# Kernel tuning notes

Hardware: AMD Instinct MI355X
Metric: run time of the kernel (lower is better)

## Reference

```python
import jax, jax.numpy as jnp
import numpy as np

VOCAB = 32000
D_MODEL = 512
SEQ_TABLE = 2048
EPS = 1e-5


def layer_norm(x, gamma, beta):
    mu = jnp.mean(x, axis=-1, keepdims=True)
    var = jnp.mean(jnp.square(x - mu), axis=-1, keepdims=True)
    return (x - mu) * jax.lax.rsqrt(var + EPS) * gamma + beta


def setup_inputs() -> dict:
    key = jax.random.key(0)
    ks = jax.random.split(key, 12)
    s = 0.02
    d, h, V = D_MODEL, 4 * D_MODEL, VOCAB
    return {
        "x": jax.random.randint(ks[0], (4, 2048), 0, V, dtype=jnp.int64),
        "word_emb": jax.random.normal(ks[1], (V, d), jnp.float32) * s,
        "pos_emb": jax.random.normal(ks[2], (SEQ_TABLE, d), jnp.float32) * s,
        "Wq": jax.random.normal(ks[3], (d, d), jnp.float32) * s,
        "Wk": jax.random.normal(ks[4], (d, d), jnp.float32) * s,
        "Wv": jax.random.normal(ks[5], (d, d), jnp.float32) * s,
        "g1": jnp.ones((d,), jnp.float32),
        "b1": jnp.zeros((d,), jnp.float32),
        "w_ffn1": jax.random.normal(ks[6], (h, d), jnp.float32) * s,
        "b_ffn1": jnp.zeros((h,), jnp.float32),
        "w_ffn2": jax.random.normal(ks[7], (d, h), jnp.float32) * s,
        "b_ffn2": jnp.zeros((d,), jnp.float32),
        "g2": jnp.ones((d,), jnp.float32),
        "b2": jnp.zeros((d,), jnp.float32),
        "w_vocab": jax.random.normal(ks[8], (V, d), jnp.float32) * s,
        "b_vocab": jnp.zeros((V,), jnp.float32),
    }


def reference(x, word_emb, pos_emb, Wq, Wk, Wv, g1, b1,
              w_ffn1, b_ffn1, w_ffn2, b_ffn2, g2, b2, w_vocab, b_vocab):
    B, S = x.shape
    d_k = Wq.shape[0]
    # embeddings: word + learned positional
    emb = word_emb[x] + pos_emb[jnp.arange(S)][None, :, :]  # [B,S,d]
    # single-head causal attention (torch Linear: y = x @ W.T)
    Q = emb @ Wq.T
    K = emb @ Wk.T
    V = emb @ Wv.T
    scores = jnp.einsum('bqd,bkd->bqk', Q, K) / jnp.sqrt(jnp.float32(d_k))
    causal = jnp.tril(jnp.ones((S, S), bool))
    scores = jnp.where(causal[None], scores, -jnp.inf)
    attn = jax.nn.softmax(scores, axis=-1)
    context = jnp.einsum('bqk,bkd->bqd', attn, V)
    out1 = layer_norm(emb + context, g1, b1)
    ffn = jax.nn.relu(out1 @ w_ffn1.T + b_ffn1) @ w_ffn2.T + b_ffn2
    final = layer_norm(out1 + ffn, g2, b2)
    return final @ w_vocab.T + b_vocab  # [B,S,V]
```

## Files before the change

kernel.cpp:

```cpp
#include <hip/hip_runtime.h>
#include <hip/hip_bf16.h>

typedef __bf16 bf16;
typedef __attribute__((ext_vector_type(4))) __bf16 bf16x4;
typedef __attribute__((ext_vector_type(8))) __bf16 bf16x8;
typedef __attribute__((ext_vector_type(4))) float f32x4;

__device__ inline void gload_lds16(const bf16* g, bf16* l) {
    __builtin_amdgcn_global_load_lds(
        (const __attribute__((address_space(1))) void*)g,
        (__attribute__((address_space(3))) void*)l, 16, 0, 0);
}

struct CvtArgs {
    const float* src[6];
    bf16* dst[6];
    long n4[6];
    float scale[6];
};
__global__ void cvt_all(CvtArgs a) {
    int j = blockIdx.y;
    const float* __restrict__ src = a.src[j];
    bf16* __restrict__ dst = a.dst[j];
    long n4 = a.n4[j];
    float sc = a.scale[j];
    long i = (long)blockIdx.x * blockDim.x + threadIdx.x;
    long stride = (long)gridDim.x * blockDim.x;
    for (; i < n4; i += stride) {
        float4 v = ((const float4*)src)[i];
        bf16x4 o = { (bf16)(v.x * sc), (bf16)(v.y * sc), (bf16)(v.z * sc), (bf16)(v.w * sc) };
        ((bf16x4*)dst)[i] = o;
    }
}

__global__ void embed_kernel(const int* __restrict__ x, const float* __restrict__ we,
                             const float* __restrict__ pe, float* __restrict__ emb_f,
                             bf16* __restrict__ emb_b) {
    int row = blockIdx.x;
    int c   = threadIdx.x;
    int tok = x[row];
    int s   = row & 2047;
    float4 w = ((const float4*)we)[(long)tok * 128 + c];
    float4 p = ((const float4*)pe)[(long)s * 128 + c];
    float4 e = { w.x + p.x, w.y + p.y, w.z + p.z, w.w + p.w };
    ((float4*)emb_f)[(long)row * 128 + c] = e;
    bf16x4 eb = { (bf16)e.x, (bf16)e.y, (bf16)e.z, (bf16)e.w };
    ((bf16x4*)emb_b)[(long)row * 128 + c] = eb;
}

template<bool WF32>
__global__ void ln_kernel(const float* __restrict__ a, const float* __restrict__ bres,
                          const float* __restrict__ g, const float* __restrict__ bb,
                          float* __restrict__ of, bf16* __restrict__ ob) {
    int row = blockIdx.x;
    int t   = threadIdx.x;
    float4 xa = ((const float4*)a)[(long)row * 128 + t];
    float4 xb = ((const float4*)bres)[(long)row * 128 + t];
    float4 xv = { xa.x + xb.x, xa.y + xb.y, xa.z + xb.z, xa.w + xb.w };
    float s  = xv.x + xv.y + xv.z + xv.w;
    float sq = xv.x * xv.x + xv.y * xv.y + xv.z * xv.z + xv.w * xv.w;
    #pragma unroll
    for (int o = 32; o > 0; o >>= 1) {
        s  += __shfl_xor(s, o);
        sq += __shfl_xor(sq, o);
    }
    __shared__ float rs[2], rq[2];
    int wid = t >> 6;
    if ((t & 63) == 0) { rs[wid] = s; rq[wid] = sq; }
    __syncthreads();
    s = rs[0] + rs[1]; sq = rq[0] + rq[1];
    float mu   = s * (1.0f / 512.0f);
    float var  = sq * (1.0f / 512.0f) - mu * mu;
    float rstd = rsqrtf(var + 1e-5f);
    float4 gv = ((const float4*)g)[t];
    float4 bv = ((const float4*)bb)[t];
    float4 y = { (xv.x - mu) * rstd * gv.x + bv.x,
                 (xv.y - mu) * rstd * gv.y + bv.y,
                 (xv.z - mu) * rstd * gv.z + bv.z,
                 (xv.w - mu) * rstd * gv.w + bv.w };
    if (WF32) ((float4*)of)[(long)row * 128 + t] = y;
    bf16x4 yb = { (bf16)y.x, (bf16)y.y, (bf16)y.z, (bf16)y.w };
    ((bf16x4*)ob)[(long)row * 128 + t] = yb;
}

__global__ void softmax_causal(const float* __restrict__ sc, bf16* __restrict__ pr) {
    int row = blockIdx.x;
    int z = row >> 11, q = row & 2047;
    const float* srow = sc + ((long)z * 2048 + q) * 2048;
    bf16*        prow = pr + ((long)z * 2048 + q) * 2048;
    int t = threadIdx.x;
    float v[8];
    int c0 = t * 8;
    if (t <= (q >> 3)) {
        float4 v0 = ((const float4*)srow)[t * 2];
        float4 v1 = ((const float4*)srow)[t * 2 + 1];
        v[0] = v0.x; v[1] = v0.y; v[2] = v0.z; v[3] = v0.w;
        v[4] = v1.x; v[5] = v1.y; v[6] = v1.z; v[7] = v1.w;
    } else {
        #pragma unroll
        for (int j = 0; j < 8; j++) v[j] = -1e30f;
    }
    float mx = -1e30f;
    #pragma unroll
    for (int j = 0; j < 8; j++) {
        if (c0 + j > q) v[j] = -1e30f;
        mx = fmaxf(mx, v[j]);
    }
    int lane = t & 63, wid = t >> 6;
    #pragma unroll
    for (int o = 32; o > 0; o >>= 1) mx = fmaxf(mx, __shfl_xor(mx, o));
    __shared__ float redm[4], reds[4];
    if (lane == 0) redm[wid] = mx;
    __syncthreads();
    mx = fmaxf(fmaxf(redm[0], redm[1]), fmaxf(redm[2], redm[3]));
    float p[8]; float sum = 0.f;
    #pragma unroll
    for (int j = 0; j < 8; j++) {
        p[j] = (c0 + j <= q) ? __expf(v[j] - mx) : 0.f;
        sum += p[j];
    }
    #pragma unroll
    for (int o = 32; o > 0; o >>= 1) sum += __shfl_xor(sum, o);
    if (lane == 0) reds[wid] = sum;
    __syncthreads();
    sum = reds[0] + reds[1] + reds[2] + reds[3];
    float inv = 1.0f / sum;
    int wlim = ((q >> 7) + 1) * 128;
    if (c0 < wlim) {
        bf16x8 o;
        #pragma unroll
        for (int j = 0; j < 8; j++) o[j] = (bf16)(p[j] * inv);
        *(bf16x8*)&prow[c0] = o;
    }
}

enum { EPI_F32 = 0, EPI_BF16 = 1, EPI_VT = 2, EPI_BIAS_RELU_BF16 = 3, EPI_BIAS_F32 = 4,
       EPI_QKV = 5, EPI_BIAS_F32_NT = 6 };
enum { ZB_BATCH = 0 };

template<int EPI, bool CAUSAL_SKIP, bool CAUSAL_K, bool XCD, int ZMODE>
__global__ __launch_bounds__(256)
void gemm_bt(const bf16* __restrict__ A, const bf16* __restrict__ B,
             float* __restrict__ Cf, bf16* __restrict__ Cb,
             const float* __restrict__ bias, float scale,
             int M, int N, int K, int Krow, long sA, long sB, long sC) {
    int br, bc;
    if (XCD) {
        int nwg = gridDim.x * gridDim.y;
        int lin = blockIdx.y * gridDim.x + blockIdx.x;
        lin = (lin & 7) * (nwg >> 3) + (lin >> 3);
        br = lin / gridDim.x; bc = lin - br * gridDim.x;
    } else { br = blockIdx.y; bc = blockIdx.x; }
    int z = blockIdx.z;
    A += (long)z * sA; B += (long)z * sB; Cf += (long)z * sC;
    if (CAUSAL_SKIP && bc > br) return;
    int Kext = CAUSAL_K ? min(K, (br + 1) * 128) : K;
    __shared__ bf16 As[128 * 64];
    __shared__ bf16 Bs[128 * 64];
    int tid = threadIdx.x;
    int lane = tid & 63, wid = tid >> 6;
    int wm = (wid >> 1) * 64, wn = (wid & 1) * 64;
    f32x4 acc[4][4] = {};
    int rowA0 = br * 128, colB0 = bc * 128;
    int rsub = lane >> 3;
    int csub = ((lane & 7) ^ rsub) * 8;
    int rdsw = (lane & 7) * 8;
    for (int kt = 0; kt < Kext; kt += 64) {
        const bf16* Ag = A + (long)rowA0 * Krow + kt;
        const bf16* Bg = B + (long)colB0 * Krow + kt;
        #pragma unroll
        for (int i = 0; i < 4; i++) {
            int seg = wid * 4 + i;
            int r = seg * 8 + rsub;
            gload_lds16(&Ag[(long)r * Krow + csub], &As[seg * 512]);
            gload_lds16(&Bg[(long)r * Krow + csub], &Bs[seg * 512]);
        }
        __syncthreads();
        #pragma unroll
        for (int kk = 0; kk < 2; kk++) {
            bf16x8 af[4], bfr[4];
            int ko = (kk * 32 + (lane >> 4) * 8) ^ rdsw;
            #pragma unroll
            for (int m = 0; m < 4; m++) af[m]  = *(const bf16x8*)&As[(wm + m * 16 + (lane & 15)) * 64 + ko];
            #pragma unroll
            for (int n = 0; n < 4; n++) bfr[n] = *(const bf16x8*)&Bs[(wn + n * 16 + (lane & 15)) * 64 + ko];
            #pragma unroll
            for (int m = 0; m < 4; m++)
                #pragma unroll
                for (int n = 0; n < 4; n++)
                    acc[m][n] = __builtin_amdgcn_mfma_f32_16x16x32_bf16(af[m], bfr[n], acc[m][n], 0, 0, 0);
        }
        __syncthreads();
    }
    #pragma unroll
    for (int m = 0; m < 4; m++) {
        #pragma unroll
        for (int n = 0; n < 4; n++) {
            #pragma unroll
            for (int j = 0; j < 4; j++) {
                int row = rowA0 + wm + m * 16 + (lane >> 4) * 4 + j;
                int col = colB0 + wn + n * 16 + (lane & 15);
                float v = acc[m][n][j];
                if (EPI == EPI_F32) {
                    Cf[(long)row * N + col] = v;
                } else if (EPI == EPI_BF16) {
                    Cb[(long)row * N + col] = (bf16)(v * scale);
                } else if (EPI == EPI_VT) {
                    int b = row >> 11, k = row & 2047;
                    Cb[((long)b * 512 + col) * 2048 + k] = (bf16)v;
                } else if (EPI == EPI_BIAS_RELU_BF16) {
                    float y = fmaxf(v + bias[col], 0.0f);
                    Cb[(long)row * N + col] = (bf16)y;
                } else if (EPI == EPI_BIAS_F32) {
                    Cf[(long)row * N + col] = v + bias[col];
                }
            }
        }
    }
}

template<int EPI, bool XCD, bool CSKIP, int BANDW, int NT>
__global__ __launch_bounds__(512)
void gemm256(const bf16* __restrict__ A, const bf16* __restrict__ B,
             float* __restrict__ Cf, bf16* __restrict__ Cb,
             const float* __restrict__ bias, int N, int K,
             long sA, long sB, long sC) {
    int br, bc;
    if (XCD) {
        int nwg = gridDim.x * gridDim.y;
        int lin = blockIdx.y * gridDim.x + blockIdx.x;
        lin = (lin & 7) * (nwg >> 3) + (lin >> 3);
        if (BANDW > 0) {
            int per = BANDW * gridDim.y;
            int band = lin / per, w2 = lin - band * per;
            br = w2 / BANDW; bc = band * BANDW + (w2 - br * BANDW);
        } else {
            br = lin / gridDim.x; bc = lin - br * gridDim.x;
        }
    } else { br = blockIdx.y; bc = blockIdx.x; }
    if (CSKIP && bc > br) return;
    int z = blockIdx.z;
    A  += (long)z * sA;
    B  += (long)z * sB;
    Cf += (long)z * sC;
    __shared__ bf16 lds[2][2][256 * 64];
    int tid = threadIdx.x;
    int lane = tid & 63, wid = tid >> 6;
    int wm2 = wid >> 2, wn4 = wid & 3;
    long rowA0 = (long)br * 256, colB0 = (long)bc * 256;
    int rsub = lane >> 3;
    int csw  = ((lane & 7) ^ rsub) * 8;
    int l15 = lane & 15;
    int rdxor = (lane & 7) << 3;
    int kbase = (lane >> 4) * 8;
    const bf16* Abase = A + rowA0 * K;
    const bf16* Bbase = B + colB0 * K;
    f32x4 acc[8][4] = {};

    auto stage = [&](int t) {
        int buf = t & 1;
        const bf16* Ag = Abase + t * 64;
        const bf16* Bg = Bbase + t * 64;
        #pragma unroll
        for (int i = 0; i < 4; i++) {
            int seg = wid * 4 + i;
            long r = seg * 8 + rsub;
            gload_lds16(&Ag[r * K + csw], &lds[buf][0][seg * 512]);
        }
        #pragma unroll
        for (int i = 0; i < 4; i++) {
            int seg = wid * 4 + i;
            long r = seg * 8 + rsub;
            gload_lds16(&Bg[r * K + csw], &lds[buf][1][seg * 512]);
        }
    };

    stage(0);
    stage(1);

    for (int t = 0; t < NT; t++) {
        int buf = t & 1;
        if (t == NT - 1) asm volatile("s_waitcnt vmcnt(0)" ::: "memory");
        else             asm volatile("s_waitcnt vmcnt(8)" ::: "memory");
        __builtin_amdgcn_s_barrier();
        const bf16* As = lds[buf][0];
        const bf16* Bs = lds[buf][1];
        bf16x8 bfr[2][4], af[2][4];
        #pragma unroll
        for (int kk = 0; kk < 2; kk++)
            #pragma unroll
            for (int n = 0; n < 4; n++) {
                int r = wn4 * 64 + n * 16 + l15;
                bfr[kk][n] = *(const bf16x8*)&Bs[r * 64 + ((kk * 32 + kbase) ^ rdxor)];
            }
        #pragma unroll
        for (int kk = 0; kk < 2; kk++)
            #pragma unroll
            for (int m = 0; m < 4; m++) {
                int r = wm2 * 128 + m * 16 + l15;
                af[kk][m] = *(const bf16x8*)&As[r * 64 + ((kk * 32 + kbase) ^ rdxor)];
            }
        __builtin_amdgcn_s_setprio(1);
        #pragma unroll
        for (int kk = 0; kk < 2; kk++)
            #pragma unroll
            for (int m = 0; m < 4; m++)
                #pragma unroll
                for (int n = 0; n < 4; n++)
                    acc[m][n] = __builtin_amdgcn_mfma_f32_16x16x32_bf16(af[kk][m], bfr[kk][n], acc[m][n], 0, 0, 0);
        __builtin_amdgcn_s_setprio(0);
        #pragma unroll
        for (int kk = 0; kk < 2; kk++)
            #pragma unroll
            for (int m = 0; m < 4; m++) {
                int r = wm2 * 128 + 64 + m * 16 + l15;
                af[kk][m] = *(const bf16x8*)&As[r * 64 + ((kk * 32 + kbase) ^ rdxor)];
            }
        asm volatile("s_waitcnt lgkmcnt(0)" ::: "memory");
        __builtin_amdgcn_sched_barrier(0);
        __builtin_amdgcn_s_barrier();
        if (t + 2 < NT) stage(t + 2);
        __builtin_amdgcn_s_setprio(1);
        #pragma unroll
        for (int kk = 0; kk < 2; kk++)
            #pragma unroll
            for (int m = 0; m < 4; m++)
                #pragma unroll
                for (int n = 0; n < 4; n++)
                    acc[4 + m][n] = __builtin_amdgcn_mfma_f32_16x16x32_bf16(af[kk][m], bfr[kk][n], acc[4 + m][n], 0, 0, 0);
        __builtin_amdgcn_s_setprio(0);
    }

    if constexpr (EPI == EPI_QKV) {
        int region = (int)(colB0 >> 9);
        if (region < 2) {
            bf16* dst = Cb + (long)region * (8192L * 512);
            int cb = ((int)colB0 & 511) + wn4 * 64;
            #pragma unroll
            for (int m = 0; m < 8; m++)
                #pragma unroll
                for (int n = 0; n < 4; n++)
                    #pragma unroll
                    for (int j = 0; j < 4; j++) {
                        long row = rowA0 + wm2 * 128 + m * 16 + (lane >> 4) * 4 + j;
                        int c = cb + n * 16 + l15;
                        dst[row * 512 + c] = (bf16)acc[m][n][j];
                    }
        } else {
            bf16* vtb = Cb + 2L * 8192 * 512;
            int cb = ((int)colB0 - 1024) + wn4 * 64;
            #pragma unroll
            for (int m = 0; m < 8; m++)
                #pragma unroll
                for (int n = 0; n < 4; n++) {
                    long k0 = rowA0 + wm2 * 128 + m * 16 + (lane >> 4) * 4;
                    long b = k0 >> 11, k = k0 & 2047;
                    int c = cb + n * 16 + l15;
                    bf16x4 pk = { (bf16)acc[m][n][0], (bf16)acc[m][n][1],
                                  (bf16)acc[m][n][2], (bf16)acc[m][n][3] };
                    *(bf16x4*)&vtb[(b * 512 + c) * 2048 + k] = pk;
                }
        }
    } else {
        #pragma unroll
        for (int m = 0; m < 8; m++) {
            #pragma unroll
            for (int n = 0; n < 4; n++) {
                #pragma unroll
                for (int j = 0; j < 4; j++) {
                    long row = rowA0 + wm2 * 128 + m * 16 + (lane >> 4) * 4 + j;
                    long col = colB0 + wn4 * 64 + n * 16 + l15;
                    float v = acc[m][n][j];
                    if (EPI == EPI_BIAS_F32) {
                        Cf[row * N + col] = v + bias[col];
                    } else if (EPI == EPI_BIAS_F32_NT) {
                        __builtin_nontemporal_store(v + bias[col], &Cf[row * N + col]);
                    } else if (EPI == EPI_BIAS_RELU_BF16) {
                        Cb[row * N + col] = (bf16)fmaxf(v + bias[col], 0.0f);
                    } else if (EPI == EPI_F32) {
                        Cf[row * N + col] = v;
                    }
                }
            }
        }
    }
}

template<int BANDB>
__global__ __launch_bounds__(256)
void gemm128v(const bf16* __restrict__ A, const bf16* __restrict__ B,
              float* __restrict__ C, const float* __restrict__ bias,
              int N, int K) {
    const int NBR = 64;
    const int NT  = 8;
    int nwg = gridDim.x;
    int lin = blockIdx.x;
    lin = (lin & 7) * (nwg >> 3) + (lin >> 3);
    int per = BANDB * NBR;
    int band = lin / per, w2 = lin - band * per;
    int br = w2 / BANDB, bc = band * BANDB + (w2 - br * BANDB);

    __shared__ bf16 lds[2][2][128 * 64];
    int tid = threadIdx.x;
    int lane = tid & 63, wid = tid >> 6;
    int wm = (wid >> 1) * 64, wn = (wid & 1) * 64;
    int rsub = lane >> 3;
    int csub = ((lane & 7) ^ rsub) * 8;
    int rdsw = (lane & 7) * 8;
    long rowA0 = (long)br * 128, colB0 = (long)bc * 128;
    const bf16* Abase = A + rowA0 * K;
    const bf16* Bbase = B + colB0 * K;
    f32x4 acc[4][4] = {};

    auto stage = [&](int t) {
        int buf = t & 1;
        const bf16* Ag = Abase + t * 64;
        const bf16* Bg = Bbase + t * 64;
        #pragma unroll
        for (int i = 0; i < 4; i++) {
            int seg = wid * 4 + i;
            long r = seg * 8 + rsub;
            gload_lds16(&Ag[r * K + csub], &lds[buf][0][seg * 512]);
        }
        #pragma unroll
        for (int i = 0; i < 4; i++) {
            int seg = wid * 4 + i;
            long r = seg * 8 + rsub;
            gload_lds16(&Bg[r * K + csub], &lds[buf][1][seg * 512]);
        }
    };

    stage(0);
    stage(1);

    for (int t = 0; t < NT; t++) {
        int buf = t & 1;
        if (t == NT - 1) asm volatile("s_waitcnt vmcnt(0)" ::: "memory");
        else             asm volatile("s_waitcnt vmcnt(8)" ::: "memory");
        __builtin_amdgcn_s_barrier();
        const bf16* As = lds[buf][0];
        const bf16* Bs = lds[buf][1];
        __builtin_amdgcn_s_setprio(1);
        #pragma unroll
        for (int kk = 0; kk < 2; kk++) {
            bf16x8 af[4], bfr[4];
            int ko = (kk * 32 + (lane >> 4) * 8) ^ rdsw;
            #pragma unroll
            for (int m = 0; m < 4; m++) af[m]  = *(const bf16x8*)&As[(wm + m * 16 + (lane & 15)) * 64 + ko];
            #pragma unroll
            for (int n = 0; n < 4; n++) bfr[n] = *(const bf16x8*)&Bs[(wn + n * 16 + (lane & 15)) * 64 + ko];
            #pragma unroll
            for (int m = 0; m < 4; m++)
                #pragma unroll
                for (int n = 0; n < 4; n++)
                    acc[m][n] = __builtin_amdgcn_mfma_f32_16x16x32_bf16(af[m], bfr[n], acc[m][n], 0, 0, 0);
        }
        __builtin_amdgcn_s_setprio(0);
        asm volatile("s_waitcnt lgkmcnt(0)" ::: "memory");
        __builtin_amdgcn_sched_barrier(0);
        __builtin_amdgcn_s_barrier();
        if (t + 2 < NT) stage(t + 2);
    }

    #pragma unroll
    for (int m = 0; m < 4; m++) {
        #pragma unroll
        for (int n = 0; n < 4; n++) {
            int col = (int)colB0 + wn + n * 16 + (lane & 15);
            float bcol = bias[col];
            #pragma unroll
            for (int j = 0; j < 4; j++) {
                long row = rowA0 + wm + m * 16 + (lane >> 4) * 4 + j;
                __builtin_nontemporal_store(acc[m][n][j] + bcol, &C[row * N + col]);
            }
        }
    }
}

extern "C" void kernel_launch(void* const* d_in, const int* in_sizes, int n_in,
                              void* d_out, int out_size, void* d_ws, size_t ws_size,
                              hipStream_t stream) {
    const int*   x       = (const int*)d_in[0];
    const float* word_emb = (const float*)d_in[1];
    const float* pos_emb  = (const float*)d_in[2];
    const float* Wq = (const float*)d_in[3];
    const float* Wk = (const float*)d_in[4];
    const float* Wv = (const float*)d_in[5];
    const float* g1 = (const float*)d_in[6];
    const float* b1 = (const float*)d_in[7];
    const float* w_ffn1 = (const float*)d_in[8];
    const float* b_ffn1 = (const float*)d_in[9];
    const float* w_ffn2 = (const float*)d_in[10];
    const float* b_ffn2 = (const float*)d_in[11];
    const float* g2 = (const float*)d_in[12];
    const float* b2 = (const float*)d_in[13];
    const float* w_vocab = (const float*)d_in[14];
    const float* b_vocab = (const float*)d_in[15];
    float* out = (float*)d_out;

    char* w = (char*)d_ws;
    auto alloc = [&](size_t bytes) { char* p = w; w += (bytes + 255) & ~255ULL; return p; };
    bf16* wqb   = (bf16*)alloc(512 * 512 * 2);
    bf16* wkb   = (bf16*)alloc(512 * 512 * 2);
    bf16* wvb   = (bf16*)alloc(512 * 512 * 2);
    bf16* w1b   = (bf16*)alloc(2048 * 512 * 2);
    bf16* w2b   = (bf16*)alloc(512 * 2048 * 2);
    bf16* wvocb = (bf16*)alloc((size_t)32000 * 512 * 2);
    float* embf = (float*)alloc((size_t)8192 * 512 * 4);
    bf16* embb  = (bf16*)alloc((size_t)8192 * 512 * 2);
    bf16* qb    = (bf16*)alloc((size_t)8192 * 512 * 2);
    bf16* kb    = (bf16*)alloc((size_t)8192 * 512 * 2);
    bf16* vt    = (bf16*)alloc((size_t)8192 * 512 * 2);
    float* scores = (float*)alloc((size_t)4 * 2048 * 2048 * 4);
    bf16* probs = (bf16*)alloc((size_t)4 * 2048 * 2048 * 2);
    float* ctx  = (float*)alloc((size_t)8192 * 512 * 4);
    float* out1f = (float*)alloc((size_t)8192 * 512 * 4);
    float* ffn2f = (float*)alloc((size_t)8192 * 512 * 4);
    bf16* ffn1b = (bf16*)scores;
    bf16* out1b = kb;
    bf16* finalb = embb;

    const float qscale = 0.044194173824159216f;

    CvtArgs ca;
    ca.src[0] = Wq;      ca.dst[0] = wqb;   ca.n4[0] = 512 * 512 / 4;          ca.scale[0] = qscale;
    ca.src[1] = Wk;      ca.dst[1] = wkb;   ca.n4[1] = 512 * 512 / 4;          ca.scale[1] = 1.0f;
    ca.src[2] = Wv;      ca.dst[2] = wvb;   ca.n4[2] = 512 * 512 / 4;          ca.scale[2] = 1.0f;
    ca.src[3] = w_ffn1;  ca.dst[3] = w1b;   ca.n4[3] = 2048 * 512 / 4;         ca.scale[3] = 1.0f;
    ca.src[4] = w_ffn2;  ca.dst[4] = w2b;   ca.n4[4] = 512 * 2048 / 4;         ca.scale[4] = 1.0f;
    ca.src[5] = w_vocab; ca.dst[5] = wvocb; ca.n4[5] = (long)32000 * 512 / 4;  ca.scale[5] = 1.0f;
    cvt_all<<<dim3(256, 6), 256, 0, stream>>>(ca);

    embed_kernel<<<8192, 128, 0, stream>>>(x, word_emb, pos_emb, embf, embb);

    gemm256<EPI_QKV, true, false, 0, 8><<<dim3(6, 32, 1), 512, 0, stream>>>(
        embb, wqb, nullptr, qb, nullptr, 1536, 512, 0, 0, 0);

    gemm256<EPI_F32, true, true, 0, 8><<<dim3(8, 8, 4), 512, 0, stream>>>(
        qb, kb, scores, nullptr, nullptr, 2048, 512,
        (long)2048 * 512, (long)2048 * 512, (long)2048 * 2048);

    softmax_causal<<<8192, 256, 0, stream>>>(scores, probs);

    gemm_bt<EPI_F32, false, true, false, ZB_BATCH><<<dim3(4, 16, 4), 256, 0, stream>>>(
        probs, vt, ctx, nullptr, nullptr, 1.0f, 2048, 512, 2048, 2048,
        (long)2048 * 2048, (long)512 * 2048, (long)2048 * 512);

    ln_kernel<true><<<8192, 128, 0, stream>>>(embf, ctx, g1, b1, out1f, out1b);

    gemm256<EPI_BIAS_RELU_BF16, true, false, 0, 8><<<dim3(8, 32, 1), 512, 0, stream>>>(
        out1b, w1b, nullptr, ffn1b, b_ffn1, 2048, 512, 0, 0, 0);

    gemm_bt<EPI_BIAS_F32, false, false, false, ZB_BATCH><<<dim3(4, 64, 1), 256, 0, stream>>>(
        ffn1b, w2b, ffn2f, nullptr, b_ffn2, 1.0f, 8192, 512, 2048, 2048, 0, 0, 0);

    ln_kernel<false><<<8192, 128, 0, stream>>>(out1f, ffn2f, g2, b2, nullptr, finalb);

    gemm128v<10><<<16000, 256, 0, stream>>>(finalb, wvocb, out, b_vocab, 32000, 512);
}
```

Measured before the change: 553.8 us.

## Split-K the PV and FFN2 GEMMs and reduce the partials in layernorm

The causal P·V GEMM is split into two K chunks of 1024. Blocks whose causal range does not reach the second chunk exit early, and the second chunk's partial sums go to a separate buffer. The FFN2 GEMM is split along K into two halves written to separate fp32 buffers, and its bias add moves out of the GEMM. The layernorm kernels now sum the residual, both partials and the bias, which doubles the block count for these small-grid GEMMs and evens out the causal load imbalance. The cost is extra fp32 partial buffers and more memory traffic in the layernorm passes.

Result: faster. 535.5 us (-3.3%).

```diff
diff --git a/kernel.cpp b/kernel.cpp
--- a/kernel.cpp
+++ b/kernel.cpp
@@ -48,15 +48,24 @@
     ((bf16x4*)emb_b)[(long)row * 128 + c] = eb;
 }
 
-template<bool WF32>
-__global__ void ln_kernel(const float* __restrict__ a, const float* __restrict__ bres,
+template<bool WF32, int C3, bool RBIAS>
+__global__ void ln_kernel(const float* __restrict__ a, const float* __restrict__ b,
+                          const float* __restrict__ c, const float* __restrict__ rb,
                           const float* __restrict__ g, const float* __restrict__ bb,
                           float* __restrict__ of, bf16* __restrict__ ob) {
     int row = blockIdx.x;
     int t   = threadIdx.x;
     float4 xa = ((const float4*)a)[(long)row * 128 + t];
-    float4 xb = ((const float4*)bres)[(long)row * 128 + t];
+    float4 xb = ((const float4*)b)[(long)row * 128 + t];
     float4 xv = { xa.x + xb.x, xa.y + xb.y, xa.z + xb.z, xa.w + xb.w };
+    if (C3 == 2 || (C3 == 1 && (row & 2047) >= 1024)) {
+        float4 xc = ((const float4*)c)[(long)row * 128 + t];
+        xv.x += xc.x; xv.y += xc.y; xv.z += xc.z; xv.w += xc.w;
+    }
+    if (RBIAS) {
+        float4 rv = ((const float4*)rb)[t];
+        xv.x += rv.x; xv.y += rv.y; xv.z += rv.z; xv.w += rv.w;
+    }
     float s  = xv.x + xv.y + xv.z + xv.w;
     float sq = xv.x * xv.x + xv.y * xv.y + xv.z * xv.z + xv.w * xv.w;
     #pragma unroll
@@ -136,7 +145,7 @@
 
 enum { EPI_F32 = 0, EPI_BF16 = 1, EPI_VT = 2, EPI_BIAS_RELU_BF16 = 3, EPI_BIAS_F32 = 4,
        EPI_QKV = 5, EPI_BIAS_F32_NT = 6 };
-enum { ZB_BATCH = 0 };
+enum { ZB_BATCH = 0, ZB_PV = 1 };
 
 template<int EPI, bool CAUSAL_SKIP, bool CAUSAL_K, bool XCD, int ZMODE>
 __global__ __launch_bounds__(256)
@@ -152,9 +161,21 @@
         br = lin / gridDim.x; bc = lin - br * gridDim.x;
     } else { br = blockIdx.y; bc = blockIdx.x; }
     int z = blockIdx.z;
-    A += (long)z * sA; B += (long)z * sB; Cf += (long)z * sC;
+    int Kext = K;
+    if (ZMODE == ZB_BATCH) {
+        A += (long)z * sA; B += (long)z * sB; Cf += (long)z * sC;
+    } else if (ZMODE == ZB_PV) {
+        int batch = z >> 1, chunk = z & 1;
+        A += (long)batch * sA; B += (long)batch * sB;
+        Cf += (long)chunk * (8192L * 512) + (long)batch * sC;
+        int keff = min(K, (br + 1) * 128);
+        int lo = chunk * 1024;
+        if (keff <= lo) return;
+        A += lo; B += lo;
+        Kext = min(keff, lo + 1024) - lo;
+    }
     if (CAUSAL_SKIP && bc > br) return;
-    int Kext = CAUSAL_K ? min(K, (br + 1) * 128) : K;
+    if (CAUSAL_K) Kext = min(Kext, (br + 1) * 128);
     __shared__ bf16 As[128 * 64];
     __shared__ bf16 Bs[128 * 64];
     int tid = threadIdx.x;
@@ -514,8 +535,10 @@
     float* scores = (float*)alloc((size_t)4 * 2048 * 2048 * 4);
     bf16* probs = (bf16*)alloc((size_t)4 * 2048 * 2048 * 2);
     float* ctx  = (float*)alloc((size_t)8192 * 512 * 4);
+    float* pv1  = (float*)alloc((size_t)8192 * 512 * 4);
     float* out1f = (float*)alloc((size_t)8192 * 512 * 4);
     float* ffn2f = (float*)alloc((size_t)8192 * 512 * 4);
+    float* ffn2b = (float*)alloc((size_t)8192 * 512 * 4);
     bf16* ffn1b = (bf16*)scores;
     bf16* out1b = kb;
     bf16* finalb = embb;
@@ -542,19 +565,22 @@
 
     softmax_causal<<<8192, 256, 0, stream>>>(scores, probs);
 
-    gemm_bt<EPI_F32, false, true, false, ZB_BATCH><<<dim3(4, 16, 4), 256, 0, stream>>>(
+    gemm_bt<EPI_F32, false, false, false, ZB_PV><<<dim3(4, 16, 8), 256, 0, stream>>>(
         probs, vt, ctx, nullptr, nullptr, 1.0f, 2048, 512, 2048, 2048,
         (long)2048 * 2048, (long)512 * 2048, (long)2048 * 512);
 
-    ln_kernel<true><<<8192, 128, 0, stream>>>(embf, ctx, g1, b1, out1f, out1b);
+    ln_kernel<true, 1, false><<<8192, 128, 0, stream>>>(
+        embf, ctx, pv1, nullptr, g1, b1, out1f, out1b);
 
     gemm256<EPI_BIAS_RELU_BF16, true, false, 0, 8><<<dim3(8, 32, 1), 512, 0, stream>>>(
         out1b, w1b, nullptr, ffn1b, b_ffn1, 2048, 512, 0, 0, 0);
 
-    gemm_bt<EPI_BIAS_F32, false, false, false, ZB_BATCH><<<dim3(4, 64, 1), 256, 0, stream>>>(
-        ffn1b, w2b, ffn2f, nullptr, b_ffn2, 1.0f, 8192, 512, 2048, 2048, 0, 0, 0);
-
-    ln_kernel<false><<<8192, 128, 0, stream>>>(out1f, ffn2f, g2, b2, nullptr, finalb);
+    gemm_bt<EPI_F32, false, false, false, ZB_BATCH><<<dim3(4, 64, 2), 256, 0, stream>>>(
+        ffn1b, w2b, ffn2f, nullptr, nullptr, 1.0f, 8192, 512, 1024, 2048,
+        1024, 1024, 8192L * 512);
+
+    ln_kernel<false, 2, true><<<8192, 128, 0, stream>>>(
+        out1f, ffn2f, ffn2b, b_ffn2, g2, b2, nullptr, finalb);
 
     gemm128v<10><<<16000, 256, 0, stream>>>(finalb, wvocb, out, b_vocab, 32000, 512);
 }
```
